# Performance work log

Hardware: AMD Instinct MI355X
Metric: run time of the kernel (lower is better)

## Reference

```python
import jax, jax.numpy as jnp
import numpy as np

EPS = 1e-5

def _conv1x1(x, w, b):
    # x: [B,C,H,W], w: [O,C], b: [O]
    return jnp.einsum('bchw,oc->bohw', x, w) + b[None, :, None, None]

def setup_inputs() -> dict:
    key = jax.random.key(0)
    ks = jax.random.split(key, 6)
    B, C, H, W = 8, 512, 64, 64
    Ck, Cv, Co = 256, 256, 512
    x = jax.random.normal(ks[0], (B, C, H, W), dtype=jnp.float32)
    Wk = jax.random.normal(ks[1], (Ck, C), dtype=jnp.float32) * 0.02
    bk = jnp.zeros((Ck,), dtype=jnp.float32)
    gamma = jnp.ones((Ck,), dtype=jnp.float32)
    beta = jnp.zeros((Ck,), dtype=jnp.float32)
    Wv = jax.random.normal(ks[2], (Cv, C), dtype=jnp.float32) * 0.02
    bv = jnp.zeros((Cv,), dtype=jnp.float32)
    Ww = jax.random.normal(ks[3], (Co, Cv), dtype=jnp.float32) * 0.02
    bw = jnp.zeros((Co,), dtype=jnp.float32)
    return {'x': x, 'Wk': Wk, 'bk': bk, 'gamma': gamma, 'beta': beta,
            'Wv': Wv, 'bv': bv, 'Ww': Ww, 'bw': bw}

def reference(x, Wk, bk, gamma, beta, Wv, bv, Ww, bw):
    B, C, H, W = x.shape
    # f_key == f_query (shared module): conv1x1 -> BN (training stats) -> ReLU
    qk = _conv1x1(x, Wk, bk)                      # [B,Ck,H,W]
    mean = qk.mean(axis=(0, 2, 3))
    var = qk.var(axis=(0, 2, 3))                  # biased variance, as torch BN training
    feat = jax.nn.relu((qk - mean[None, :, None, None])
                       * jax.lax.rsqrt(var + EPS)[None, :, None, None]
                       * gamma[None, :, None, None] + beta[None, :, None, None])
    value = _conv1x1(x, Wv, bv)                   # [B,Cv,H,W]
    Ck = feat.shape[1]
    Cv = value.shape[1]
    N = H * W
    q = feat.reshape(B, Ck, N).transpose(0, 2, 1)  # [B,N,Ck]
    k = feat.reshape(B, Ck, N)                     # [B,Ck,N]
    v = value.reshape(B, Cv, N).transpose(0, 2, 1) # [B,N,Cv]
    scale = Ck ** (-0.5)
    sim = jax.nn.softmax(jnp.matmul(q, k) * scale, axis=-1)  # [B,N,N]
    ctx = jnp.matmul(sim, v)                       # [B,N,Cv]
    ctx = ctx.transpose(0, 2, 1).reshape(B, Cv, H, W)
    out = _conv1x1(ctx, Ww, bw)                    # [B,Co,H,W]
    # scale==1 -> visualize_* upsamples are identity; sim_map visual is None
    return (out, feat, feat, value)
```

## Files before the change

kernel.cpp:

```cpp
#include <hip/hip_runtime.h>
#include <math.h>

constexpr int  Bn  = 8;
constexpr int  Cin = 512;
constexpr int  Nn  = 4096;
constexpr int  Ck  = 256;
constexpr int  Cv  = 256;
constexpr int  Co  = 512;

constexpr size_t F1_OFF  = (size_t)Bn * Co * Nn;
constexpr size_t F2_OFF  = F1_OFF + (size_t)Bn * Ck * Nn;
constexpr size_t VAL_OFF = F2_OFF + (size_t)Bn * Ck * Nn;

typedef __attribute__((ext_vector_type(8)))  short  short8;
typedef __attribute__((ext_vector_type(16))) float  f32x16;
typedef __attribute__((ext_vector_type(8)))  ushort ushort8;

static __device__ __forceinline__ ushort f2bf(float f) {
    union { float f; unsigned u; } x; x.f = f;
    unsigned r = x.u + 0x7fffu + ((x.u >> 16) & 1u);
    return (ushort)(r >> 16);
}

static __device__ __forceinline__ void gll16(const void* g, void* l) {
    __builtin_amdgcn_global_load_lds(
        (const __attribute__((address_space(1))) void*)g,
        (__attribute__((address_space(3))) void*)l, 16, 0, 0);
}

__global__ __launch_bounds__(256) void cast_w(const float* __restrict__ a,
                                              const float* __restrict__ b,
                                              const float* __restrict__ c,
                                              ushort* __restrict__ da,
                                              ushort* __restrict__ db,
                                              ushort* __restrict__ dc)
{
    const int tid   = blockIdx.x * 256 + threadIdx.x;
    const int which = tid >> 14;
    const int off   = (tid & 16383) * 8;
    const float* s = (which == 0) ? a : (which == 1) ? b : c;
    ushort*      d = (which == 0) ? da : (which == 1) ? db : dc;
    const float4 u = *(const float4*)(s + off);
    const float4 v = *(const float4*)(s + off + 4);
    ushort8 o;
    o[0] = f2bf(u.x); o[1] = f2bf(u.y); o[2] = f2bf(u.z); o[3] = f2bf(u.w);
    o[4] = f2bf(v.x); o[5] = f2bf(v.y); o[6] = f2bf(v.z); o[7] = f2bf(v.w);
    *(ushort8*)(d + off) = o;
}

__global__ __launch_bounds__(256) void transpose_c(const float* __restrict__ src,
                                                   ushort* __restrict__ dst, int C)
{
    const int b  = blockIdx.z;
    const int c0 = blockIdx.y * 64;
    const int n0 = blockIdx.x * 64;
    const int t  = threadIdx.x;
    __shared__ float T[64][65];
#pragma unroll
    for (int p = 0; p < 4; ++p) {
        const int flat = p * 256 + t;
        const int cc = flat >> 4, nn4 = (flat & 15) * 4;
        const float4 v = *(const float4*)(
            src + ((size_t)b * C + c0 + cc) * Nn + n0 + nn4);
        T[cc][nn4]     = v.x; T[cc][nn4 + 1] = v.y;
        T[cc][nn4 + 2] = v.z; T[cc][nn4 + 3] = v.w;
    }
    __syncthreads();
#pragma unroll
    for (int p = 0; p < 2; ++p) {
        const int flat = p * 256 + t;
        const int nn = flat >> 3, cc0 = (flat & 7) * 8;
        ushort8 o;
#pragma unroll
        for (int i = 0; i < 8; ++i) o[i] = f2bf(T[cc0 + i][nn]);
        *(ushort8*)(dst + ((size_t)b * Nn + n0 + nn) * C + c0 + cc0) = o;
    }
}

__global__ __launch_bounds__(256) void gemm_qv(const ushort* __restrict__ XT,
                                               const ushort* __restrict__ Wkb,
                                               const ushort* __restrict__ Wvb,
                                               const float*  __restrict__ bk,
                                               const float*  __restrict__ bv,
                                               float* __restrict__ qk,
                                               float* __restrict__ val,
                                               ushort* __restrict__ valB)
{
    const int b  = blockIdx.z;
    const int m0 = blockIdx.y * 128;
    const int n0 = blockIdx.x * 128;
    const int t  = threadIdx.x;
    const int w  = t >> 6, L = t & 63;
    const int l31 = L & 31, hl = L >> 5;
    const int wm = (w >> 1) * 64, wn = (w & 1) * 64;

    __shared__ __align__(16) short AsK[128][72];
    __shared__ __align__(16) short AsV[128][72];
    __shared__ __align__(16) short Bs[128][72];

    const ushort* Xb = XT + (size_t)b * Nn * Cin;

    f32x16 accK[2][2], accV[2][2];
#pragma unroll
    for (int a = 0; a < 2; ++a)
#pragma unroll
        for (int bb = 0; bb < 2; ++bb)
#pragma unroll
            for (int r = 0; r < 16; ++r) { accK[a][bb][r] = 0.f; accV[a][bb][r] = 0.f; }

    for (int k0 = 0; k0 < Cin; k0 += 64) {
        __syncthreads();
#pragma unroll
        for (int p = 0; p < 4; ++p) {
            const int e   = p * 256 + t;
            const int row = e >> 3, ko = (e & 7) * 8;
            *(short8*)&AsK[row][ko] =
                *(const short8*)(Wkb + (size_t)(m0 + row) * Cin + k0 + ko);
            *(short8*)&AsV[row][ko] =
                *(const short8*)(Wvb + (size_t)(m0 + row) * Cin + k0 + ko);
            *(short8*)&Bs[row][ko] =
                *(const short8*)(Xb + (size_t)(n0 + row) * Cin + k0 + ko);
        }
        __syncthreads();
#pragma unroll
        for (int kc = 0; kc < 4; ++kc) {
            short8 Ak[2], Av[2], Bf[2];
#pragma unroll
            for (int a = 0; a < 2; ++a) {
                Ak[a] = *(const short8*)&AsK[wm + a * 32 + l31][kc * 16 + hl * 8];
                Av[a] = *(const short8*)&AsV[wm + a * 32 + l31][kc * 16 + hl * 8];
            }
#pragma unroll
            for (int bb = 0; bb < 2; ++bb)
                Bf[bb] = *(const short8*)&Bs[wn + bb * 32 + l31][kc * 16 + hl * 8];
#pragma unroll
            for (int a = 0; a < 2; ++a)
#pragma unroll
                for (int bb = 0; bb < 2; ++bb) {
                    accK[a][bb] = __builtin_amdgcn_mfma_f32_32x32x16_bf16(
                        Ak[a], Bf[bb], accK[a][bb], 0, 0, 0);
                    accV[a][bb] = __builtin_amdgcn_mfma_f32_32x32x16_bf16(
                        Av[a], Bf[bb], accV[a][bb], 0, 0, 0);
                }
        }
    }

#pragma unroll
    for (int a = 0; a < 2; ++a)
#pragma unroll
        for (int r = 0; r < 16; ++r) {
            const int row = (r & 3) + 8 * (r >> 2) + 4 * hl;
            const int o   = m0 + wm + a * 32 + row;
            const float bkv = bk[o], bvv = bv[o];
            const size_t base = ((size_t)b * Ck + o) * Nn + n0 + wn + l31;
#pragma unroll
            for (int bb = 0; bb < 2; ++bb) {
                qk[base + bb * 32] = accK[a][bb][r] + bkv;
                const float vv = accV[a][bb][r] + bvv;
                val[base + bb * 32]  = vv;
                valB[base + bb * 32] = f2bf(vv);
            }
        }
}

__global__ __launch_bounds__(256) void bn_stats(const float* __restrict__ qk,
                                                const float* __restrict__ gamma,
                                                const float* __restrict__ beta,
                                                float* __restrict__ ss)
{
    const int o = blockIdx.x;
    const int t = threadIdx.x;
    float s = 0.f, sq = 0.f;
    for (int b = 0; b < Bn; ++b) {
        const float* p = qk + ((size_t)b * Ck + o) * Nn;
        for (int n = t * 4; n < Nn; n += 1024) {
            const float4 v = *(const float4*)(p + n);
            s  += v.x + v.y + v.z + v.w;
            sq += v.x * v.x + v.y * v.y + v.z * v.z + v.w * v.w;
        }
    }
    __shared__ float rs[256], rq[256];
    rs[t] = s; rq[t] = sq;
    __syncthreads();
    for (int off = 128; off > 0; off >>= 1) {
        if (t < off) { rs[t] += rs[t + off]; rq[t] += rq[t + off]; }
        __syncthreads();
    }
    if (t == 0) {
        const float cnt  = (float)(Bn * Nn);
        const float mean = rs[0] / cnt;
        const float var  = rq[0] / cnt - mean * mean;
        const float inv  = rsqrtf(var + 1e-5f);
        const float sc   = gamma[o] * inv;
        ss[o]       = sc;
        ss[256 + o] = beta[o] - mean * sc;
    }
}

__global__ __launch_bounds__(256) void bn_relu_t(const float* __restrict__ qk,
                                                 const float* __restrict__ ss,
                                                 float* __restrict__ f1,
                                                 float* __restrict__ f2,
                                                 ushort* __restrict__ featT)
{
    const int b  = blockIdx.z;
    const int c0 = blockIdx.y * 64;
    const int n0 = blockIdx.x * 64;
    const int t  = threadIdx.x;
    __shared__ float T[64][65];
#pragma unroll
    for (int p = 0; p < 4; ++p) {
        const int flat = p * 256 + t;
        const int cc = flat >> 4, nn4 = (flat & 15) * 4;
        const size_t gidx = ((size_t)b * Ck + c0 + cc) * Nn + n0 + nn4;
        const float sc = ss[c0 + cc], sh = ss[256 + c0 + cc];
        const float4 v = *(const float4*)(qk + gidx);
        float4 r;
        r.x = fmaxf(v.x * sc + sh, 0.f);
        r.y = fmaxf(v.y * sc + sh, 0.f);
        r.z = fmaxf(v.z * sc + sh, 0.f);
        r.w = fmaxf(v.w * sc + sh, 0.f);
        *(float4*)(f1 + gidx) = r;
        *(float4*)(f2 + gidx) = r;
        T[cc][nn4]     = r.x; T[cc][nn4 + 1] = r.y;
        T[cc][nn4 + 2] = r.z; T[cc][nn4 + 3] = r.w;
    }
    __syncthreads();
#pragma unroll
    for (int p = 0; p < 2; ++p) {
        const int flat = p * 256 + t;
        const int nn = flat >> 3, cc0 = (flat & 7) * 8;
        ushort8 o;
#pragma unroll
        for (int i = 0; i < 8; ++i) o[i] = f2bf(T[cc0 + i][nn]);
        *(ushort8*)(featT + ((size_t)b * Nn + n0 + nn) * Ck + c0 + cc0) = o;
    }
}

constexpr int LDS_BYTES = 163840;

__global__ __launch_bounds__(512) void attn_mfma(const ushort* __restrict__ featT,
                                                 const ushort* __restrict__ valB,
                                                 ushort* __restrict__ ctx)
{
    extern __shared__ __align__(16) char lds[];
    char* ldsK = lds;
    char* ldsV = lds + 65536;
    char* ldsP = lds + 131072;

    const int b   = blockIdx.x;
    const int i0  = blockIdx.y * 128;
    const int t   = threadIdx.x;
    const int w   = t >> 6;
    const int L   = t & 63;
    const int l31 = L & 31, hl = L >> 5;
    const int ig  = w >> 1;
    const int ch  = w & 1;
    const int jsel = ch * 32;

    const int rbK  = hl * 16 + (((jsel + l31) << 4) & 511);
    const int rotV = (l31 << 4) & 127;

    const ushort* F = featT + (size_t)b * Nn * Ck;
    const ushort* V = valB  + (size_t)b * Cv * Nn;
    const char*   Vg = (const char*)V;

    constexpr float CEXP = 0.09016844005556021f;
    constexpr int NT = Nn / 64;

#define STAGE_K(J0, BUF) do {                                                  \
        const char* Kg_ = (const char*)(F + (size_t)(J0) * Ck);                \
        char* Kd_ = ldsK + (BUF) * 32768;                                      \
        _Pragma("unroll")                                                      \
        for (int p_ = 0; p_ < 4; ++p_) {                                       \
            const int c_ = w * 4 + p_;                                         \
            const int o_ = c_ * 1024 + L * 16;                                 \
            const int rK_ = o_ >> 9;                                           \
            gll16(Kg_ + rK_ * 512 + ((o_ - rK_ * 16) & 511), Kd_ + c_ * 1024); \
        }                                                                      \
    } while (0)

#define STAGE_V(J0, BUF) do {                                                  \
        char* Vd_ = ldsV + (BUF) * 32768;                                      \
        _Pragma("unroll")                                                      \
        for (int p_ = 0; p_ < 4; ++p_) {                                       \
            const int c_ = w * 4 + p_;                                         \
            const int o_ = c_ * 1024 + L * 16;                                 \
            const int rV_ = o_ >> 7;                                           \
            gll16(Vg + (size_t)rV_ * (Nn * 2) + (size_t)(J0) * 2               \
                     + ((o_ - rV_ * 16) & 127), Vd_ + c_ * 1024);              \
        }                                                                      \
    } while (0)

    STAGE_K(0, 0);
    short8 Qf[16];
    {
        const ushort* qp = F + ((size_t)(i0 + ig * 32 + l31)) * Ck + hl * 8;
#pragma unroll
        for (int kc = 0; kc < 16; ++kc)
            Qf[kc] = *(const short8*)(qp + kc * 16);
    }
    asm volatile("s_waitcnt vmcnt(0)" ::: "memory");
    __builtin_amdgcn_s_barrier();

    f32x16 Oacc[4];
#pragma unroll
    for (int c = 0; c < 4; ++c)
#pragma unroll
        for (int r = 0; r < 16; ++r) Oacc[c][r] = 0.f;
    float lsum = 0.f;

    int cur = 0;
    for (int s = 0; s < NT; ++s) {
        const int jn = (s + 1 < NT ? s + 1 : NT - 1) * 64;
        STAGE_K(jn, cur ^ 1);
        STAGE_V((size_t)s * 64, cur);

        const char* Kr = ldsK + cur * 32768 + (jsel + l31) * 512;
        f32x16 Sa, Sb;
#pragma unroll
        for (int r = 0; r < 16; ++r) { Sa[r] = 0.f; Sb[r] = 0.f; }
        __builtin_amdgcn_s_setprio(1);
#pragma unroll
        for (int kc = 0; kc < 8; ++kc) {
            const short8 K0 = *(const short8*)(Kr + ((kc * 64      + rbK) & 511));
            const short8 K1 = *(const short8*)(Kr + ((kc * 64 + 32 + rbK) & 511));
            Sa = __builtin_amdgcn_mfma_f32_32x32x16_bf16(K0, Qf[2 * kc],     Sa, 0, 0, 0);
            Sb = __builtin_amdgcn_mfma_f32_32x32x16_bf16(K1, Qf[2 * kc + 1], Sb, 0, 0, 0);
        }
        __builtin_amdgcn_s_setprio(0);

        if (s > 0) {
            const char* Vr2 = ldsV + (cur ^ 1) * 32768 + (ch * 128 + l31) * 128;
            const char* Pr  = ldsP + (cur ^ 1) * 16384 + (ig * 8 + hl) * 512 + l31 * 16;
            __builtin_amdgcn_s_setprio(1);
#pragma unroll
            for (int jb = 0; jb < 4; ++jb) {
                const short8 Pa = *(const short8*)(Pr + jb * 1024);
                const int jbyte = jb * 32 + hl * 16;
#pragma unroll
                for (int cvt = 0; cvt < 4; ++cvt) {
                    const short8 Vf = *(const short8*)(Vr2 + cvt * 4096
                                         + ((jbyte + rotV) & 127));
                    Oacc[cvt] = __builtin_amdgcn_mfma_f32_32x32x16_bf16(
                        Pa, Vf, Oacc[cvt], 0, 0, 0);
                }
            }
            __builtin_amdgcn_s_setprio(0);
        }

        unsigned pw[8];
#pragma unroll
        for (int r2 = 0; r2 < 8; ++r2) {
            const float p0 = exp2f((Sa[2 * r2]     + Sb[2 * r2])     * CEXP);
            const float p1 = exp2f((Sa[2 * r2 + 1] + Sb[2 * r2 + 1]) * CEXP);
            lsum += p0 + p1;
            unsigned pk;
            asm("v_cvt_pk_bf16_f32 %0, %1, %2" : "=v"(pk) : "v"(p0), "v"(p1));
            pw[r2] = pk;
        }
        {
            char* Pw = ldsP + cur * 16384
                       + ((ig * 4 + ch * 2) * 2 + hl) * 512 + l31 * 16;
#pragma unroll
            for (int g = 0; g < 2; ++g) {
                auto s02 = __builtin_amdgcn_permlane32_swap(pw[4 * g + 0], pw[4 * g + 2],
                                                            false, false);
                auto s13 = __builtin_amdgcn_permlane32_swap(pw[4 * g + 1], pw[4 * g + 3],
                                                            false, false);
                union { unsigned u[4]; short8 s; } pu;
                pu.u[0] = s02[0]; pu.u[1] = s13[0]; pu.u[2] = s02[1]; pu.u[3] = s13[1];
                *(short8*)(Pw + g * 1024) = pu.s;
            }
        }

        asm volatile("s_waitcnt vmcnt(0) lgkmcnt(0)" ::: "memory");
        __builtin_amdgcn_s_barrier();
        cur ^= 1;
    }
#undef STAGE_K
#undef STAGE_V

    {
        const char* Vr2 = ldsV + (cur ^ 1) * 32768 + (ch * 128 + l31) * 128;
        const char* Pr  = ldsP + (cur ^ 1) * 16384 + (ig * 8 + hl) * 512 + l31 * 16;
#pragma unroll
        for (int jb = 0; jb < 4; ++jb) {
            const short8 Pa = *(const short8*)(Pr + jb * 1024);
            const int jbyte = jb * 32 + hl * 16;
#pragma unroll
            for (int cvt = 0; cvt < 4; ++cvt) {
                const short8 Vf = *(const short8*)(Vr2 + cvt * 4096
                                     + ((jbyte + rotV) & 127));
                Oacc[cvt] = __builtin_amdgcn_mfma_f32_32x32x16_bf16(
                    Pa, Vf, Oacc[cvt], 0, 0, 0);
            }
        }
    }

    {
        unsigned a = __float_as_uint(lsum), bcopy = a;
        auto sw = __builtin_amdgcn_permlane32_swap(a, bcopy, false, false);
        lsum = __uint_as_float(sw[0]) + __uint_as_float(sw[1]);
    }
    float* Lr = (float*)ldsP;
    Lr[(ig * 2 + ch) * 32 + l31] = lsum;
    asm volatile("s_waitcnt lgkmcnt(0)" ::: "memory");
    __builtin_amdgcn_s_barrier();

    ushort* Cb = ctx + ((size_t)b * Nn + i0 + ig * 32) * Cv + ch * 128;
#pragma unroll
    for (int r = 0; r < 16; ++r) {
        const int row = (r & 3) + 8 * (r >> 2) + 4 * hl;
        const float lt = Lr[(ig * 2) * 32 + row] + Lr[(ig * 2 + 1) * 32 + row];
        const float linv = 1.f / lt;
        ushort* cp = Cb + (size_t)row * Cv + l31;
#pragma unroll
        for (int c4 = 0; c4 < 4; ++c4)
            cp[c4 * 32] = f2bf(Oacc[c4][r] * linv);
    }
}

template <int K>
__global__ __launch_bounds__(256) void gemm_bf(const ushort* __restrict__ XT,
                                               const ushort* __restrict__ Wb,
                                               const float*  __restrict__ bias,
                                               float* __restrict__ out,
                                               int M)
{
    const int b  = blockIdx.z;
    const int m0 = blockIdx.y * 128;
    const int n0 = blockIdx.x * 128;
    const int t  = threadIdx.x;
    const int w  = t >> 6, L = t & 63;
    const int l31 = L & 31, hl = L >> 5;
    const int wm = (w >> 1) * 64, wn = (w & 1) * 64;

    __shared__ __align__(16) short As[128][72];
    __shared__ __align__(16) short Bs[128][72];

    const ushort* Xb = XT + (size_t)b * Nn * K;

    f32x16 acc[2][2];
#pragma unroll
    for (int a = 0; a < 2; ++a)
#pragma unroll
        for (int bb = 0; bb < 2; ++bb)
#pragma unroll
            for (int r = 0; r < 16; ++r) acc[a][bb][r] = 0.f;

    for (int k0 = 0; k0 < K; k0 += 64) {
        __syncthreads();
#pragma unroll
        for (int p = 0; p < 4; ++p) {
            const int e   = p * 256 + t;
            const int row = e >> 3, ko = (e & 7) * 8;
            *(short8*)&As[row][ko] =
                *(const short8*)(Wb + (size_t)(m0 + row) * K + k0 + ko);
            *(short8*)&Bs[row][ko] =
                *(const short8*)(Xb + (size_t)(n0 + row) * K + k0 + ko);
        }
        __syncthreads();
#pragma unroll
        for (int kc = 0; kc < 4; ++kc) {
            short8 Af[2], Bf[2];
#pragma unroll
            for (int a = 0; a < 2; ++a)
                Af[a] = *(const short8*)&As[wm + a * 32 + l31][kc * 16 + hl * 8];
#pragma unroll
            for (int bb = 0; bb < 2; ++bb)
                Bf[bb] = *(const short8*)&Bs[wn + bb * 32 + l31][kc * 16 + hl * 8];
#pragma unroll
            for (int a = 0; a < 2; ++a)
#pragma unroll
                for (int bb = 0; bb < 2; ++bb)
                    acc[a][bb] = __builtin_amdgcn_mfma_f32_32x32x16_bf16(
                        Af[a], Bf[bb], acc[a][bb], 0, 0, 0);
        }
    }

#pragma unroll
    for (int a = 0; a < 2; ++a)
#pragma unroll
        for (int r = 0; r < 16; ++r) {
            const int row = (r & 3) + 8 * (r >> 2) + 4 * hl;
            const int o   = m0 + wm + a * 32 + row;
            const float bv = bias[o];
            const size_t base = ((size_t)b * M + o) * Nn + n0 + wn + l31;
#pragma unroll
            for (int bb = 0; bb < 2; ++bb)
                out[base + bb * 32] = acc[a][bb][r] + bv;
        }
}

extern "C" void kernel_launch(void* const* d_in, const int* in_sizes, int n_in,
                              void* d_out, int out_size, void* d_ws, size_t ws_size,
                              hipStream_t stream)
{
    const float* x     = (const float*)d_in[0];
    const float* Wk    = (const float*)d_in[1];
    const float* bk    = (const float*)d_in[2];
    const float* gamma = (const float*)d_in[3];
    const float* beta  = (const float*)d_in[4];
    const float* Wv    = (const float*)d_in[5];
    const float* bv    = (const float*)d_in[6];
    const float* Ww    = (const float*)d_in[7];
    const float* bw    = (const float*)d_in[8];

    float* out = (float*)d_out;
    float* f1  = out + F1_OFF;
    float* f2  = out + F2_OFF;
    float* val = out + VAL_OFF;

    ushort* xT    = (ushort*)d_ws;
    ushort* featT = xT;
    ushort* ctxb  = xT + (size_t)8388608;
    ushort* valB  = xT + (size_t)16777216;
    ushort* Wkb   = valB + (size_t)8388608;
    ushort* Wvb   = Wkb + 131072;
    ushort* Wwb   = Wvb + 131072;
    float*  ss    = (float*)(Wwb + 131072);

    static bool attn_attr_set = false;
    if (!attn_attr_set) {
        (void)hipFuncSetAttribute((const void*)attn_mfma,
                                  hipFuncAttributeMaxDynamicSharedMemorySize,
                                  LDS_BYTES);
        attn_attr_set = true;
    }

    cast_w<<<192, 256, 0, stream>>>(Wk, Wv, Ww, Wkb, Wvb, Wwb);
    transpose_c<<<dim3(Nn / 64, Cin / 64, Bn), 256, 0, stream>>>(x, xT, Cin);
    gemm_qv<<<dim3(Nn / 128, Ck / 128, Bn), 256, 0, stream>>>(
        xT, Wkb, Wvb, bk, bv, f1, val, valB);
    bn_stats<<<Ck, 256, 0, stream>>>(f1, gamma, beta, ss);
    bn_relu_t<<<dim3(Nn / 64, Ck / 64, Bn), 256, 0, stream>>>(
        f1, ss, f1, f2, featT);
    attn_mfma<<<dim3(Bn, Nn / 128), 512, LDS_BYTES, stream>>>(featT, valB, ctxb);
    gemm_bf<256><<<dim3(Nn / 128, Co / 128, Bn), 256, 0, stream>>>(
        ctxb, Wwb, bw, out, Co);
}
```

Measured before the change: 438.1 us.

## Fuse BN statistics into QV GEMM epilogue and retile attention PV warps

```diff
diff --git a/kernel.cpp b/kernel.cpp
--- a/kernel.cpp
+++ b/kernel.cpp
@@ -33,9 +33,11 @@
                                               const float* __restrict__ c,
                                               ushort* __restrict__ da,
                                               ushort* __restrict__ db,
-                                              ushort* __restrict__ dc)
+                                              ushort* __restrict__ dc,
+                                              float* __restrict__ ss)
 {
     const int tid   = blockIdx.x * 256 + threadIdx.x;
+    if (tid < 512) ss[tid] = 0.f;
     const int which = tid >> 14;
     const int off   = (tid & 16383) * 8;
     const float* s = (which == 0) ? a : (which == 1) ? b : c;
@@ -84,7 +86,8 @@
                                                const float*  __restrict__ bv,
                                                float* __restrict__ qk,
                                                float* __restrict__ val,
-                                               ushort* __restrict__ valB)
+                                               ushort* __restrict__ valB,
+                                               float* __restrict__ ss)
 {
     const int b  = blockIdx.z;
     const int m0 = blockIdx.y * 128;
@@ -153,52 +156,34 @@
             const int o   = m0 + wm + a * 32 + row;
             const float bkv = bk[o], bvv = bv[o];
             const size_t base = ((size_t)b * Ck + o) * Nn + n0 + wn + l31;
-#pragma unroll
-            for (int bb = 0; bb < 2; ++bb) {
-                qk[base + bb * 32] = accK[a][bb][r] + bkv;
-                const float vv = accV[a][bb][r] + bvv;
-                val[base + bb * 32]  = vv;
-                valB[base + bb * 32] = f2bf(vv);
+            const float q0 = accK[a][0][r] + bkv;
+            const float q1 = accK[a][1][r] + bkv;
+            qk[base]      = q0;
+            qk[base + 32] = q1;
+            const float v0 = accV[a][0][r] + bvv;
+            const float v1 = accV[a][1][r] + bvv;
+            val[base]       = v0;
+            val[base + 32]  = v1;
+            valB[base]      = f2bf(v0);
+            valB[base + 32] = f2bf(v1);
+            float sp = q0 + q1;
+            float qp = q0 * q0 + q1 * q1;
+#pragma unroll
+            for (int m = 1; m <= 16; m <<= 1) {
+                sp += __shfl_xor(sp, m, 64);
+                qp += __shfl_xor(qp, m, 64);
             }
-        }
-}
-
-__global__ __launch_bounds__(256) void bn_stats(const float* __restrict__ qk,
-                                                const float* __restrict__ gamma,
-                                                const float* __restrict__ beta,
-                                                float* __restrict__ ss)
-{
-    const int o = blockIdx.x;
-    const int t = threadIdx.x;
-    float s = 0.f, sq = 0.f;
-    for (int b = 0; b < Bn; ++b) {
-        const float* p = qk + ((size_t)b * Ck + o) * Nn;
-        for (int n = t * 4; n < Nn; n += 1024) {
-            const float4 v = *(const float4*)(p + n);
-            s  += v.x + v.y + v.z + v.w;
-            sq += v.x * v.x + v.y * v.y + v.z * v.z + v.w * v.w;
-        }
-    }
-    __shared__ float rs[256], rq[256];
-    rs[t] = s; rq[t] = sq;
-    __syncthreads();
-    for (int off = 128; off > 0; off >>= 1) {
-        if (t < off) { rs[t] += rs[t + off]; rq[t] += rq[t + off]; }
-        __syncthreads();
-    }
-    if (t == 0) {
-        const float cnt  = (float)(Bn * Nn);
-        const float mean = rs[0] / cnt;
-        const float var  = rq[0] / cnt - mean * mean;
-        const float inv  = rsqrtf(var + 1e-5f);
-        const float sc   = gamma[o] * inv;
-        ss[o]       = sc;
-        ss[256 + o] = beta[o] - mean * sc;
-    }
+            if (l31 == 0) {
+                atomicAdd(&ss[o], sp);
+                atomicAdd(&ss[Ck + o], qp);
+            }
+        }
 }
 
 __global__ __launch_bounds__(256) void bn_relu_t(const float* __restrict__ qk,
-                                                 const float* __restrict__ ss,
+                                                 const float* __restrict__ ssv,
+                                                 const float* __restrict__ gamma,
+                                                 const float* __restrict__ beta,
                                                  float* __restrict__ f1,
                                                  float* __restrict__ f2,
                                                  ushort* __restrict__ featT)
@@ -207,13 +192,19 @@
     const int c0 = blockIdx.y * 64;
     const int n0 = blockIdx.x * 64;
     const int t  = threadIdx.x;
+    constexpr float RCNT = 1.f / (float)(Bn * Nn);
     __shared__ float T[64][65];
 #pragma unroll
     for (int p = 0; p < 4; ++p) {
         const int flat = p * 256 + t;
         const int cc = flat >> 4, nn4 = (flat & 15) * 4;
-        const size_t gidx = ((size_t)b * Ck + c0 + cc) * Nn + n0 + nn4;
-        const float sc = ss[c0 + cc], sh = ss[256 + c0 + cc];
+        const int c = c0 + cc;
+        const size_t gidx = ((size_t)b * Ck + c) * Nn + n0 + nn4;
+        const float mean = ssv[c] * RCNT;
+        const float var  = ssv[Ck + c] * RCNT - mean * mean;
+        const float inv  = rsqrtf(var + 1e-5f);
+        const float sc   = gamma[c] * inv;
+        const float sh   = beta[c] - mean * sc;
         const float4 v = *(const float4*)(qk + gidx);
         float4 r;
         r.x = fmaxf(v.x * sc + sh, 0.f);
@@ -256,6 +247,8 @@
     const int l31 = L & 31, hl = L >> 5;
     const int ig  = w >> 1;
     const int ch  = w & 1;
+    const int iq  = w >> 2;
+    const int cq  = w & 3;
     const int jsel = ch * 32;
 
     const int rbK  = hl * 16 + (((jsel + l31) << 4) & 511);
@@ -331,19 +324,24 @@
         __builtin_amdgcn_s_setprio(0);
 
         if (s > 0) {
-            const char* Vr2 = ldsV + (cur ^ 1) * 32768 + (ch * 128 + l31) * 128;
-            const char* Pr  = ldsP + (cur ^ 1) * 16384 + (ig * 8 + hl) * 512 + l31 * 16;
+            const char* Vb2 = ldsV + (cur ^ 1) * 32768 + (cq * 64 + l31) * 128;
+            const char* Pb  = ldsP + (cur ^ 1) * 16384 + hl * 512 + l31 * 16;
             __builtin_amdgcn_s_setprio(1);
 #pragma unroll
             for (int jb = 0; jb < 4; ++jb) {
-                const short8 Pa = *(const short8*)(Pr + jb * 1024);
+                short8 Pa[2];
+#pragma unroll
+                for (int iA = 0; iA < 2; ++iA)
+                    Pa[iA] = *(const short8*)(Pb + ((iq * 2 + iA) * 4 + jb) * 1024);
                 const int jbyte = jb * 32 + hl * 16;
 #pragma unroll
-                for (int cvt = 0; cvt < 4; ++cvt) {
-                    const short8 Vf = *(const short8*)(Vr2 + cvt * 4096
+                for (int cvB = 0; cvB < 2; ++cvB) {
+                    const short8 Vf = *(const short8*)(Vb2 + cvB * 4096
                                          + ((jbyte + rotV) & 127));
-                    Oacc[cvt] = __builtin_amdgcn_mfma_f32_32x32x16_bf16(
-                        Pa, Vf, Oacc[cvt], 0, 0, 0);
+#pragma unroll
+                    for (int iA = 0; iA < 2; ++iA)
+                        Oacc[iA * 2 + cvB] = __builtin_amdgcn_mfma_f32_32x32x16_bf16(
+                            Pa[iA], Vf, Oacc[iA * 2 + cvB], 0, 0, 0);
                 }
             }
             __builtin_amdgcn_s_setprio(0);
@@ -382,18 +380,23 @@
 #undef STAGE_V
 
     {
-        const char* Vr2 = ldsV + (cur ^ 1) * 32768 + (ch * 128 + l31) * 128;
-        const char* Pr  = ldsP + (cur ^ 1) * 16384 + (ig * 8 + hl) * 512 + l31 * 16;
+        const char* Vb2 = ldsV + (cur ^ 1) * 32768 + (cq * 64 + l31) * 128;
+        const char* Pb  = ldsP + (cur ^ 1) * 16384 + hl * 512 + l31 * 16;
 #pragma unroll
         for (int jb = 0; jb < 4; ++jb) {
-            const short8 Pa = *(const short8*)(Pr + jb * 1024);
+            short8 Pa[2];
+#pragma unroll
+            for (int iA = 0; iA < 2; ++iA)
+                Pa[iA] = *(const short8*)(Pb + ((iq * 2 + iA) * 4 + jb) * 1024);
             const int jbyte = jb * 32 + hl * 16;
 #pragma unroll
-            for (int cvt = 0; cvt < 4; ++cvt) {
-                const short8 Vf = *(const short8*)(Vr2 + cvt * 4096
+            for (int cvB = 0; cvB < 2; ++cvB) {
+                const short8 Vf = *(const short8*)(Vb2 + cvB * 4096
                                      + ((jbyte + rotV) & 127));
-                Oacc[cvt] = __builtin_amdgcn_mfma_f32_32x32x16_bf16(
-                    Pa, Vf, Oacc[cvt], 0, 0, 0);
+#pragma unroll
+                for (int iA = 0; iA < 2; ++iA)
+                    Oacc[iA * 2 + cvB] = __builtin_amdgcn_mfma_f32_32x32x16_bf16(
+                        Pa[iA], Vf, Oacc[iA * 2 + cvB], 0, 0, 0);
             }
         }
     }
@@ -408,16 +411,20 @@
     asm volatile("s_waitcnt lgkmcnt(0)" ::: "memory");
     __builtin_amdgcn_s_barrier();
 
-    ushort* Cb = ctx + ((size_t)b * Nn + i0 + ig * 32) * Cv + ch * 128;
-#pragma unroll
-    for (int r = 0; r < 16; ++r) {
-        const int row = (r & 3) + 8 * (r >> 2) + 4 * hl;
-        const float lt = Lr[(ig * 2) * 32 + row] + Lr[(ig * 2 + 1) * 32 + row];
-        const float linv = 1.f / lt;
-        ushort* cp = Cb + (size_t)row * Cv + l31;
-#pragma unroll
-        for (int c4 = 0; c4 < 4; ++c4)
-            cp[c4 * 32] = f2bf(Oacc[c4][r] * linv);
+    ushort* Cb = ctx + ((size_t)b * Nn + i0 + iq * 64) * Cv + cq * 64;
+#pragma unroll
+    for (int iA = 0; iA < 2; ++iA) {
+        const int IG = iq * 2 + iA;
+#pragma unroll
+        for (int r = 0; r < 16; ++r) {
+            const int row = (r & 3) + 8 * (r >> 2) + 4 * hl;
+            const float lt = Lr[(IG * 2) * 32 + row] + Lr[(IG * 2 + 1) * 32 + row];
+            const float linv = 1.f / lt;
+            ushort* cp = Cb + (size_t)(iA * 32 + row) * Cv + l31;
+#pragma unroll
+            for (int cvB = 0; cvB < 2; ++cvB)
+                cp[cvB * 32] = f2bf(Oacc[iA * 2 + cvB][r] * linv);
+        }
     }
 }
 
@@ -529,13 +536,12 @@
         attn_attr_set = true;
     }
 
-    cast_w<<<192, 256, 0, stream>>>(Wk, Wv, Ww, Wkb, Wvb, Wwb);
+    cast_w<<<192, 256, 0, stream>>>(Wk, Wv, Ww, Wkb, Wvb, Wwb, ss);
     transpose_c<<<dim3(Nn / 64, Cin / 64, Bn), 256, 0, stream>>>(x, xT, Cin);
     gemm_qv<<<dim3(Nn / 128, Ck / 128, Bn), 256, 0, stream>>>(
-        xT, Wkb, Wvb, bk, bv, f1, val, valB);
-    bn_stats<<<Ck, 256, 0, stream>>>(f1, gamma, beta, ss);
+        xT, Wkb, Wvb, bk, bv, f1, val, valB, ss);
     bn_relu_t<<<dim3(Nn / 64, Ck / 64, Bn), 256, 0, stream>>>(
-        f1, ss, f1, f2, featT);
+        f1, ss, gamma, beta, f1, f2, featT);
     attn_mfma<<<dim3(Bn, Nn / 128), 512, LDS_BYTES, stream>>>(featT, valB, ctxb);
     gemm_bf<256><<<dim3(Nn / 128, Co / 128, Bn), 256, 0, stream>>>(
         ctxb, Wwb, bw, out, Co);
```

Result: slower. 530.4 us (+21.1%).

## Shrink attention block to 64 query rows and drop LDS double buffering

Applied to the files above, without the earlier changes.

```diff
diff --git a/kernel.cpp b/kernel.cpp
--- a/kernel.cpp
+++ b/kernel.cpp
@@ -237,25 +237,27 @@
     }
 }
 
-constexpr int LDS_BYTES = 163840;
-
-__global__ __launch_bounds__(512) void attn_mfma(const ushort* __restrict__ featT,
-                                                 const ushort* __restrict__ valB,
-                                                 ushort* __restrict__ ctx)
+constexpr int LDS_BYTES = 74240;
+
+__global__ __launch_bounds__(256, 2) void attn_mfma(const ushort* __restrict__ featT,
+                                                    const ushort* __restrict__ valB,
+                                                    ushort* __restrict__ ctx)
 {
     extern __shared__ __align__(16) char lds[];
     char* ldsK = lds;
-    char* ldsV = lds + 65536;
-    char* ldsP = lds + 131072;
+    char* ldsV = lds + 32768;
+    char* ldsP = lds + 65536;
+    float* Lr  = (float*)(lds + 73728);
 
     const int b   = blockIdx.x;
-    const int i0  = blockIdx.y * 128;
+    const int i0  = blockIdx.y * 64;
     const int t   = threadIdx.x;
     const int w   = t >> 6;
     const int L   = t & 63;
     const int l31 = L & 31, hl = L >> 5;
     const int ig  = w >> 1;
     const int ch  = w & 1;
+    const int cq  = w;
     const int jsel = ch * 32;
 
     const int rbK  = hl * 16 + (((jsel + l31) << 4) & 511);
@@ -263,36 +265,10 @@
 
     const ushort* F = featT + (size_t)b * Nn * Ck;
     const ushort* V = valB  + (size_t)b * Cv * Nn;
-    const char*   Vg = (const char*)V;
 
     constexpr float CEXP = 0.09016844005556021f;
     constexpr int NT = Nn / 64;
 
-#define STAGE_K(J0, BUF) do {                                                  \
-        const char* Kg_ = (const char*)(F + (size_t)(J0) * Ck);                \
-        char* Kd_ = ldsK + (BUF) * 32768;                                      \
-        _Pragma("unroll")                                                      \
-        for (int p_ = 0; p_ < 4; ++p_) {                                       \
-            const int c_ = w * 4 + p_;                                         \
-            const int o_ = c_ * 1024 + L * 16;                                 \
-            const int rK_ = o_ >> 9;                                           \
-            gll16(Kg_ + rK_ * 512 + ((o_ - rK_ * 16) & 511), Kd_ + c_ * 1024); \
-        }                                                                      \
-    } while (0)
-
-#define STAGE_V(J0, BUF) do {                                                  \
-        char* Vd_ = ldsV + (BUF) * 32768;                                      \
-        _Pragma("unroll")                                                      \
-        for (int p_ = 0; p_ < 4; ++p_) {                                       \
-            const int c_ = w * 4 + p_;                                         \
-            const int o_ = c_ * 1024 + L * 16;                                 \
-            const int rV_ = o_ >> 7;                                           \
-            gll16(Vg + (size_t)rV_ * (Nn * 2) + (size_t)(J0) * 2               \
-                     + ((o_ - rV_ * 16) & 127), Vd_ + c_ * 1024);              \
-        }                                                                      \
-    } while (0)
-
-    STAGE_K(0, 0);
     short8 Qf[16];
     {
         const ushort* qp = F + ((size_t)(i0 + ig * 32 + l31)) * Ck + hl * 8;
@@ -300,8 +276,6 @@
         for (int kc = 0; kc < 16; ++kc)
             Qf[kc] = *(const short8*)(qp + kc * 16);
     }
-    asm volatile("s_waitcnt vmcnt(0)" ::: "memory");
-    __builtin_amdgcn_s_barrier();
 
     f32x16 Oacc[4];
 #pragma unroll
@@ -310,13 +284,27 @@
         for (int r = 0; r < 16; ++r) Oacc[c][r] = 0.f;
     float lsum = 0.f;
 
-    int cur = 0;
-    for (int s = 0; s < NT; ++s) {
-        const int jn = (s + 1 < NT ? s + 1 : NT - 1) * 64;
-        STAGE_K(jn, cur ^ 1);
-        STAGE_V((size_t)s * 64, cur);
-
-        const char* Kr = ldsK + cur * 32768 + (jsel + l31) * 512;
+    const char* KgBase = (const char*)F;
+    const char* VgBase = (const char*)V;
+
+    for (int jt = 0; jt < NT; ++jt) {
+#pragma unroll
+        for (int p = 0; p < 8; ++p) {
+            const int o  = (p * 256 + t) * 16;
+            const int rK = o >> 9;
+            gll16(KgBase + rK * 512 + ((o - rK * 16) & 511), ldsK + o);
+        }
+#pragma unroll
+        for (int p = 0; p < 8; ++p) {
+            const int o  = (p * 256 + t) * 16;
+            const int rV = o >> 7;
+            gll16(VgBase + (size_t)rV * (Nn * 2) + ((o - rV * 16) & 127),
+                  ldsV + o);
+        }
+        asm volatile("s_waitcnt vmcnt(0)" ::: "memory");
+        __builtin_amdgcn_s_barrier();
+
+        const char* Kr = ldsK + (jsel + l31) * 512;
         f32x16 Sa, Sb;
 #pragma unroll
         for (int r = 0; r < 16; ++r) { Sa[r] = 0.f; Sb[r] = 0.f; }
@@ -329,25 +317,6 @@
             Sb = __builtin_amdgcn_mfma_f32_32x32x16_bf16(K1, Qf[2 * kc + 1], Sb, 0, 0, 0);
         }
         __builtin_amdgcn_s_setprio(0);
-
-        if (s > 0) {
-            const char* Vr2 = ldsV + (cur ^ 1) * 32768 + (ch * 128 + l31) * 128;
-            const char* Pr  = ldsP + (cur ^ 1) * 16384 + (ig * 8 + hl) * 512 + l31 * 16;
-            __builtin_amdgcn_s_setprio(1);
-#pragma unroll
-            for (int jb = 0; jb < 4; ++jb) {
-                const short8 Pa = *(const short8*)(Pr + jb * 1024);
-                const int jbyte = jb * 32 + hl * 16;
-#pragma unroll
-                for (int cvt = 0; cvt < 4; ++cvt) {
-                    const short8 Vf = *(const short8*)(Vr2 + cvt * 4096
-                                         + ((jbyte + rotV) & 127));
-                    Oacc[cvt] = __builtin_amdgcn_mfma_f32_32x32x16_bf16(
-                        Pa, Vf, Oacc[cvt], 0, 0, 0);
-                }
-            }
-            __builtin_amdgcn_s_setprio(0);
-        }
 
         unsigned pw[8];
 #pragma unroll
@@ -360,8 +329,7 @@
             pw[r2] = pk;
         }
         {
-            char* Pw = ldsP + cur * 16384
-                       + ((ig * 4 + ch * 2) * 2 + hl) * 512 + l31 * 16;
+            char* Pw = ldsP + ((ig * 4 + ch * 2) * 2 + hl) * 512 + l31 * 16;
 #pragma unroll
             for (int g = 0; g < 2; ++g) {
                 auto s02 = __builtin_amdgcn_permlane32_swap(pw[4 * g + 0], pw[4 * g + 2],
@@ -373,29 +341,37 @@
                 *(short8*)(Pw + g * 1024) = pu.s;
             }
         }
-
-        asm volatile("s_waitcnt vmcnt(0) lgkmcnt(0)" ::: "memory");
+        asm volatile("s_waitcnt lgkmcnt(0)" ::: "memory");
         __builtin_amdgcn_s_barrier();
-        cur ^= 1;
-    }
-#undef STAGE_K
-#undef STAGE_V
-
-    {
-        const char* Vr2 = ldsV + (cur ^ 1) * 32768 + (ch * 128 + l31) * 128;
-        const char* Pr  = ldsP + (cur ^ 1) * 16384 + (ig * 8 + hl) * 512 + l31 * 16;
-#pragma unroll
-        for (int jb = 0; jb < 4; ++jb) {
-            const short8 Pa = *(const short8*)(Pr + jb * 1024);
-            const int jbyte = jb * 32 + hl * 16;
-#pragma unroll
-            for (int cvt = 0; cvt < 4; ++cvt) {
-                const short8 Vf = *(const short8*)(Vr2 + cvt * 4096
-                                     + ((jbyte + rotV) & 127));
-                Oacc[cvt] = __builtin_amdgcn_mfma_f32_32x32x16_bf16(
-                    Pa, Vf, Oacc[cvt], 0, 0, 0);
+
+        {
+            const char* Vb2 = ldsV + (cq * 64 + l31) * 128;
+            const char* Pb  = ldsP + hl * 512 + l31 * 16;
+            __builtin_amdgcn_s_setprio(1);
+#pragma unroll
+            for (int jb = 0; jb < 4; ++jb) {
+                short8 Pa[2];
+#pragma unroll
+                for (int iA = 0; iA < 2; ++iA)
+                    Pa[iA] = *(const short8*)(Pb + (iA * 4 + jb) * 1024);
+                const int jbyte = jb * 32 + hl * 16;
+#pragma unroll
+                for (int cvB = 0; cvB < 2; ++cvB) {
+                    const short8 Vf = *(const short8*)(Vb2 + cvB * 4096
+                                         + ((jbyte + rotV) & 127));
+#pragma unroll
+                    for (int iA = 0; iA < 2; ++iA)
+                        Oacc[iA * 2 + cvB] = __builtin_amdgcn_mfma_f32_32x32x16_bf16(
+                            Pa[iA], Vf, Oacc[iA * 2 + cvB], 0, 0, 0);
+                }
             }
-        }
+            __builtin_amdgcn_s_setprio(0);
+        }
+        asm volatile("s_waitcnt lgkmcnt(0)" ::: "memory");
+        __builtin_amdgcn_s_barrier();
+
+        KgBase += 32768;
+        VgBase += 128;
     }
 
     {
@@ -403,21 +379,23 @@
         auto sw = __builtin_amdgcn_permlane32_swap(a, bcopy, false, false);
         lsum = __uint_as_float(sw[0]) + __uint_as_float(sw[1]);
     }
-    float* Lr = (float*)ldsP;
     Lr[(ig * 2 + ch) * 32 + l31] = lsum;
     asm volatile("s_waitcnt lgkmcnt(0)" ::: "memory");
     __builtin_amdgcn_s_barrier();
 
-    ushort* Cb = ctx + ((size_t)b * Nn + i0 + ig * 32) * Cv + ch * 128;
-#pragma unroll
-    for (int r = 0; r < 16; ++r) {
-        const int row = (r & 3) + 8 * (r >> 2) + 4 * hl;
-        const float lt = Lr[(ig * 2) * 32 + row] + Lr[(ig * 2 + 1) * 32 + row];
-        const float linv = 1.f / lt;
-        ushort* cp = Cb + (size_t)row * Cv + l31;
-#pragma unroll
-        for (int c4 = 0; c4 < 4; ++c4)
-            cp[c4 * 32] = f2bf(Oacc[c4][r] * linv);
+    ushort* Cb = ctx + ((size_t)b * Nn + i0) * Cv + cq * 64;
+#pragma unroll
+    for (int iA = 0; iA < 2; ++iA) {
+#pragma unroll
+        for (int r = 0; r < 16; ++r) {
+            const int row = (r & 3) + 8 * (r >> 2) + 4 * hl;
+            const float lt = Lr[(iA * 2) * 32 + row] + Lr[(iA * 2 + 1) * 32 + row];
+            const float linv = 1.f / lt;
+            ushort* cp = Cb + (size_t)(iA * 32 + row) * Cv + l31;
+#pragma unroll
+            for (int cvB = 0; cvB < 2; ++cvB)
+                cp[cvB * 32] = f2bf(Oacc[iA * 2 + cvB][r] * linv);
+        }
     }
 }
 
@@ -536,7 +514,7 @@
     bn_stats<<<Ck, 256, 0, stream>>>(f1, gamma, beta, ss);
     bn_relu_t<<<dim3(Nn / 64, Ck / 64, Bn), 256, 0, stream>>>(
         f1, ss, f1, f2, featT);
-    attn_mfma<<<dim3(Bn, Nn / 128), 512, LDS_BYTES, stream>>>(featT, valB, ctxb);
+    attn_mfma<<<dim3(Bn, Nn / 64), 256, LDS_BYTES, stream>>>(featT, valB, ctxb);
     gemm_bf<256><<<dim3(Nn / 128, Co / 128, Bn), 256, 0, stream>>>(
         ctxb, Wwb, bw, out, Co);
 }
```

Result: slower. 459.2 us (+4.8%).

## Use direct global-to-LDS loads with swizzle in GEMMs; retile attention PV per warp

Applied to the files above, without the earlier changes.

```diff
diff --git a/kernel.cpp b/kernel.cpp
--- a/kernel.cpp
+++ b/kernel.cpp
@@ -86,6 +86,11 @@
                                                float* __restrict__ val,
                                                ushort* __restrict__ valB)
 {
+    __shared__ __align__(16) char smem[49152];
+    char* AsK = smem;
+    char* AsV = smem + 16384;
+    char* Bs  = smem + 32768;
+
     const int b  = blockIdx.z;
     const int m0 = blockIdx.y * 128;
     const int n0 = blockIdx.x * 128;
@@ -94,11 +99,9 @@
     const int l31 = L & 31, hl = L >> 5;
     const int wm = (w >> 1) * 64, wn = (w & 1) * 64;
 
-    __shared__ __align__(16) short AsK[128][72];
-    __shared__ __align__(16) short AsV[128][72];
-    __shared__ __align__(16) short Bs[128][72];
-
-    const ushort* Xb = XT + (size_t)b * Nn * Cin;
+    const char* WkG = (const char*)(Wkb + (size_t)m0 * Cin);
+    const char* WvG = (const char*)(Wvb + (size_t)m0 * Cin);
+    const char* XbG = (const char*)(XT + ((size_t)b * Nn + n0) * Cin);
 
     f32x16 accK[2][2], accV[2][2];
 #pragma unroll
@@ -110,29 +113,34 @@
 
     for (int k0 = 0; k0 < Cin; k0 += 64) {
         __syncthreads();
+        const int kb = k0 * 2;
 #pragma unroll
         for (int p = 0; p < 4; ++p) {
-            const int e   = p * 256 + t;
-            const int row = e >> 3, ko = (e & 7) * 8;
-            *(short8*)&AsK[row][ko] =
-                *(const short8*)(Wkb + (size_t)(m0 + row) * Cin + k0 + ko);
-            *(short8*)&AsV[row][ko] =
-                *(const short8*)(Wvb + (size_t)(m0 + row) * Cin + k0 + ko);
-            *(short8*)&Bs[row][ko] =
-                *(const short8*)(Xb + (size_t)(n0 + row) * Cin + k0 + ko);
-        }
+            const int o   = (p * 256 + t) * 16;
+            const int row = o >> 7;
+            const int src = kb + ((o - (row << 4)) & 127);
+            gll16(WkG + (size_t)row * 1024 + src, AsK + o);
+            gll16(WvG + (size_t)row * 1024 + src, AsV + o);
+            gll16(XbG + (size_t)row * 1024 + src, Bs  + o);
+        }
+        asm volatile("s_waitcnt vmcnt(0)" ::: "memory");
         __syncthreads();
 #pragma unroll
         for (int kc = 0; kc < 4; ++kc) {
             short8 Ak[2], Av[2], Bf[2];
 #pragma unroll
             for (int a = 0; a < 2; ++a) {
-                Ak[a] = *(const short8*)&AsK[wm + a * 32 + l31][kc * 16 + hl * 8];
-                Av[a] = *(const short8*)&AsV[wm + a * 32 + l31][kc * 16 + hl * 8];
-            }
-#pragma unroll
-            for (int bb = 0; bb < 2; ++bb)
-                Bf[bb] = *(const short8*)&Bs[wn + bb * 32 + l31][kc * 16 + hl * 8];
+                const int row = wm + a * 32 + l31;
+                const int off = (kc * 32 + hl * 16 + (row << 4)) & 127;
+                Ak[a] = *(const short8*)(AsK + row * 128 + off);
+                Av[a] = *(const short8*)(AsV + row * 128 + off);
+            }
+#pragma unroll
+            for (int bb = 0; bb < 2; ++bb) {
+                const int row = wn + bb * 32 + l31;
+                const int off = (kc * 32 + hl * 16 + (row << 4)) & 127;
+                Bf[bb] = *(const short8*)(Bs + row * 128 + off);
+            }
 #pragma unroll
             for (int a = 0; a < 2; ++a)
 #pragma unroll
@@ -237,7 +245,7 @@
     }
 }
 
-constexpr int LDS_BYTES = 163840;
+constexpr int ATTN_LDS_BYTES = 163840;
 
 __global__ __launch_bounds__(512) void attn_mfma(const ushort* __restrict__ featT,
                                                  const ushort* __restrict__ valB,
@@ -256,6 +264,8 @@
     const int l31 = L & 31, hl = L >> 5;
     const int ig  = w >> 1;
     const int ch  = w & 1;
+    const int iq  = w >> 2;
+    const int cq  = w & 3;
     const int jsel = ch * 32;
 
     const int rbK  = hl * 16 + (((jsel + l31) << 4) & 511);
@@ -331,19 +341,24 @@
         __builtin_amdgcn_s_setprio(0);
 
         if (s > 0) {
-            const char* Vr2 = ldsV + (cur ^ 1) * 32768 + (ch * 128 + l31) * 128;
-            const char* Pr  = ldsP + (cur ^ 1) * 16384 + (ig * 8 + hl) * 512 + l31 * 16;
+            const char* Vb2 = ldsV + (cur ^ 1) * 32768 + (cq * 64 + l31) * 128;
+            const char* Pb  = ldsP + (cur ^ 1) * 16384 + hl * 512 + l31 * 16;
             __builtin_amdgcn_s_setprio(1);
 #pragma unroll
             for (int jb = 0; jb < 4; ++jb) {
-                const short8 Pa = *(const short8*)(Pr + jb * 1024);
+                short8 Pa[2];
+#pragma unroll
+                for (int iA = 0; iA < 2; ++iA)
+                    Pa[iA] = *(const short8*)(Pb + ((iq * 2 + iA) * 4 + jb) * 1024);
                 const int jbyte = jb * 32 + hl * 16;
 #pragma unroll
-                for (int cvt = 0; cvt < 4; ++cvt) {
-                    const short8 Vf = *(const short8*)(Vr2 + cvt * 4096
+                for (int cvB = 0; cvB < 2; ++cvB) {
+                    const short8 Vf = *(const short8*)(Vb2 + cvB * 4096
                                          + ((jbyte + rotV) & 127));
-                    Oacc[cvt] = __builtin_amdgcn_mfma_f32_32x32x16_bf16(
-                        Pa, Vf, Oacc[cvt], 0, 0, 0);
+#pragma unroll
+                    for (int iA = 0; iA < 2; ++iA)
+                        Oacc[iA * 2 + cvB] = __builtin_amdgcn_mfma_f32_32x32x16_bf16(
+                            Pa[iA], Vf, Oacc[iA * 2 + cvB], 0, 0, 0);
                 }
             }
             __builtin_amdgcn_s_setprio(0);
@@ -382,18 +397,23 @@
 #undef STAGE_V
 
     {
-        const char* Vr2 = ldsV + (cur ^ 1) * 32768 + (ch * 128 + l31) * 128;
-        const char* Pr  = ldsP + (cur ^ 1) * 16384 + (ig * 8 + hl) * 512 + l31 * 16;
+        const char* Vb2 = ldsV + (cur ^ 1) * 32768 + (cq * 64 + l31) * 128;
+        const char* Pb  = ldsP + (cur ^ 1) * 16384 + hl * 512 + l31 * 16;
 #pragma unroll
         for (int jb = 0; jb < 4; ++jb) {
-            const short8 Pa = *(const short8*)(Pr + jb * 1024);
+            short8 Pa[2];
+#pragma unroll
+            for (int iA = 0; iA < 2; ++iA)
+                Pa[iA] = *(const short8*)(Pb + ((iq * 2 + iA) * 4 + jb) * 1024);
             const int jbyte = jb * 32 + hl * 16;
 #pragma unroll
-            for (int cvt = 0; cvt < 4; ++cvt) {
-                const short8 Vf = *(const short8*)(Vr2 + cvt * 4096
+            for (int cvB = 0; cvB < 2; ++cvB) {
+                const short8 Vf = *(const short8*)(Vb2 + cvB * 4096
                                      + ((jbyte + rotV) & 127));
-                Oacc[cvt] = __builtin_amdgcn_mfma_f32_32x32x16_bf16(
-                    Pa, Vf, Oacc[cvt], 0, 0, 0);
+#pragma unroll
+                for (int iA = 0; iA < 2; ++iA)
+                    Oacc[iA * 2 + cvB] = __builtin_amdgcn_mfma_f32_32x32x16_bf16(
+                        Pa[iA], Vf, Oacc[iA * 2 + cvB], 0, 0, 0);
             }
         }
     }
@@ -408,16 +428,20 @@
     asm volatile("s_waitcnt lgkmcnt(0)" ::: "memory");
     __builtin_amdgcn_s_barrier();
 
-    ushort* Cb = ctx + ((size_t)b * Nn + i0 + ig * 32) * Cv + ch * 128;
-#pragma unroll
-    for (int r = 0; r < 16; ++r) {
-        const int row = (r & 3) + 8 * (r >> 2) + 4 * hl;
-        const float lt = Lr[(ig * 2) * 32 + row] + Lr[(ig * 2 + 1) * 32 + row];
-        const float linv = 1.f / lt;
-        ushort* cp = Cb + (size_t)row * Cv + l31;
-#pragma unroll
-        for (int c4 = 0; c4 < 4; ++c4)
-            cp[c4 * 32] = f2bf(Oacc[c4][r] * linv);
+    ushort* Cb = ctx + ((size_t)b * Nn + i0 + iq * 64) * Cv + cq * 64;
+#pragma unroll
+    for (int iA = 0; iA < 2; ++iA) {
+        const int IG = iq * 2 + iA;
+#pragma unroll
+        for (int r = 0; r < 16; ++r) {
+            const int row = (r & 3) + 8 * (r >> 2) + 4 * hl;
+            const float lt = Lr[(IG * 2) * 32 + row] + Lr[(IG * 2 + 1) * 32 + row];
+            const float linv = 1.f / lt;
+            ushort* cp = Cb + (size_t)(iA * 32 + row) * Cv + l31;
+#pragma unroll
+            for (int cvB = 0; cvB < 2; ++cvB)
+                cp[cvB * 32] = f2bf(Oacc[iA * 2 + cvB][r] * linv);
+        }
     }
 }
 
@@ -428,6 +452,10 @@
                                                float* __restrict__ out,
                                                int M)
 {
+    __shared__ __align__(16) char smem[32768];
+    char* As = smem;
+    char* Bs = smem + 16384;
+
     const int b  = blockIdx.z;
     const int m0 = blockIdx.y * 128;
     const int n0 = blockIdx.x * 128;
@@ -436,10 +464,9 @@
     const int l31 = L & 31, hl = L >> 5;
     const int wm = (w >> 1) * 64, wn = (w & 1) * 64;
 
-    __shared__ __align__(16) short As[128][72];
-    __shared__ __align__(16) short Bs[128][72];
-
-    const ushort* Xb = XT + (size_t)b * Nn * K;
+    const char* WG = (const char*)(Wb + (size_t)m0 * K);
+    const char* XG = (const char*)(XT + ((size_t)b * Nn + n0) * K);
+    constexpr int RSTRIDE = K * 2;
 
     f32x16 acc[2][2];
 #pragma unroll
@@ -451,25 +478,32 @@
 
     for (int k0 = 0; k0 < K; k0 += 64) {
         __syncthreads();
+        const int kb = k0 * 2;
 #pragma unroll
         for (int p = 0; p < 4; ++p) {
-            const int e   = p * 256 + t;
-            const int row = e >> 3, ko = (e & 7) * 8;
-            *(short8*)&As[row][ko] =
-                *(const short8*)(Wb + (size_t)(m0 + row) * K + k0 + ko);
-            *(short8*)&Bs[row][ko] =
-                *(const short8*)(Xb + (size_t)(n0 + row) * K + k0 + ko);
-        }
+            const int o   = (p * 256 + t) * 16;
+            const int row = o >> 7;
+            const int src = kb + ((o - (row << 4)) & 127);
+            gll16(WG + (size_t)row * RSTRIDE + src, As + o);
+            gll16(XG + (size_t)row * RSTRIDE + src, Bs + o);
+        }
+        asm volatile("s_waitcnt vmcnt(0)" ::: "memory");
         __syncthreads();
 #pragma unroll
         for (int kc = 0; kc < 4; ++kc) {
             short8 Af[2], Bf[2];
 #pragma unroll
-            for (int a = 0; a < 2; ++a)
-                Af[a] = *(const short8*)&As[wm + a * 32 + l31][kc * 16 + hl * 8];
-#pragma unroll
-            for (int bb = 0; bb < 2; ++bb)
-                Bf[bb] = *(const short8*)&Bs[wn + bb * 32 + l31][kc * 16 + hl * 8];
+            for (int a = 0; a < 2; ++a) {
+                const int row = wm + a * 32 + l31;
+                const int off = (kc * 32 + hl * 16 + (row << 4)) & 127;
+                Af[a] = *(const short8*)(As + row * 128 + off);
+            }
+#pragma unroll
+            for (int bb = 0; bb < 2; ++bb) {
+                const int row = wn + bb * 32 + l31;
+                const int off = (kc * 32 + hl * 16 + (row << 4)) & 127;
+                Bf[bb] = *(const short8*)(Bs + row * 128 + off);
+            }
 #pragma unroll
             for (int a = 0; a < 2; ++a)
 #pragma unroll
@@ -525,7 +559,7 @@
     if (!attn_attr_set) {
         (void)hipFuncSetAttribute((const void*)attn_mfma,
                                   hipFuncAttributeMaxDynamicSharedMemorySize,
-                                  LDS_BYTES);
+                                  ATTN_LDS_BYTES);
         attn_attr_set = true;
     }
 
@@ -536,7 +570,7 @@
     bn_stats<<<Ck, 256, 0, stream>>>(f1, gamma, beta, ss);
     bn_relu_t<<<dim3(Nn / 64, Ck / 64, Bn), 256, 0, stream>>>(
         f1, ss, f1, f2, featT);
-    attn_mfma<<<dim3(Bn, Nn / 128), 512, LDS_BYTES, stream>>>(featT, valB, ctxb);
+    attn_mfma<<<dim3(Bn, Nn / 128), 512, ATTN_LDS_BYTES, stream>>>(featT, valB, ctxb);
     gemm_bf<256><<<dim3(Nn / 128, Co / 128, Bn), 256, 0, stream>>>(
         ctxb, Wwb, bw, out, Co);
 }
```

New measurement: 444.4 us. About the same (+1.4%).
